# Kernel optimization log

Measured on AMD Instinct MI355X. Metric: run time of the kernel, lower is better.

The kernel has to match this reference:

```python
import jax, jax.numpy as jnp
import numpy as np

GROUPS = 9  # hardcoded in GTLModuleV1.forward


def setup_inputs() -> dict:
    key = jax.random.key(0)
    k1, k2, k3 = jax.random.split(key, 3)
    B, C, N, K = 4, 144, 16384, 16
    queryandkey = jax.random.normal(k1, (B, C, N), dtype=jnp.float32)
    value = jax.random.normal(k2, (B, C, N), dtype=jnp.float32)
    idx_knn = jax.random.randint(k3, (B, N, K), 0, N, dtype=jnp.int32)
    return {"queryandkey": queryandkey, "value": value, "idx_knn": idx_knn}


def _gather_neighbours(x, idx_flat, B, G, d, N, K):
    # x: (B, G, d, N); idx_flat: (B, 1, 1, N*K) -> (B, G, d, N, K)
    g = jnp.take_along_axis(x, jnp.broadcast_to(idx_flat, (B, G, d, N * K)), axis=3)
    return g.reshape(B, G, d, N, K)


def reference(queryandkey, value, idx_knn):
    B, C, N = queryandkey.shape
    K = idx_knn.shape[-1]
    G = GROUPS
    d = C // G  # Cl = C (Cnl = 0 in GTLModuleV1)

    q = queryandkey.reshape(B, G, d, N)          # LocalQuery == LocalKey source
    v = value.reshape(B, G, d, N)
    idx_flat = idx_knn.reshape(B, 1, 1, N * K)

    key_g = _gather_neighbours(q, idx_flat, B, G, d, N, K)  # (B,G,d,N,K)
    val_g = _gather_neighbours(v, idx_flat, B, G, d, N, K)  # (B,G,d,N,K)

    # LocalAtt = sum_d Q * K_gathered, softmax over neighbors
    att = jnp.einsum('bgdn,bgdnk->bgnk', q, key_g)
    att = jax.nn.softmax(att, axis=-1)                       # (B,G,N,K)

    # attention centrality: scatter_add of attention weights onto neighbor ids
    cent = jnp.zeros((B, G, N), dtype=att.dtype).at[
        jnp.arange(B)[:, None, None, None],
        jnp.arange(G)[None, :, None, None],
        idx_knn[:, None, :, :],
    ].add(att)                                               # (B,G,N)

    # weighted aggregation of gathered values
    feat = jnp.einsum('bgnk,bgdnk->bgdn', att, val_g).reshape(B, C, N)
    return feat, cent
```

## Files before the change

kernel.cpp:

```cpp
#include <hip/hip_runtime.h>
#include <hip/hip_fp16.h>

#define BATCH 4
#define CHAN  144
#define NPTS  16384
#define KNN   16
#define GRP   9
#define DIM   16
#define ROWU  (GRP * DIM)
#define PCHUNK 21
#define NPAIR (BATCH * GRP)

#define TT 32

typedef __attribute__((ext_vector_type(2))) _Float16 h2v;
typedef __attribute__((ext_vector_type(4))) float    f4v;
typedef __attribute__((ext_vector_type(4))) int      i4v;
typedef __attribute__((ext_vector_type(4))) unsigned u4v;
__device__ __forceinline__ h2v as_h2(unsigned int u) {
  union { unsigned int u; h2v h; } c; c.u = u; return c.h;
}
__device__ __forceinline__ float2 h2f(unsigned u) {
  union { unsigned u; __half2 h; } c; c.u = u;
  return __half22float2(c.h);
}

template<int J>
__device__ __forceinline__ int ibcast(int v) {
  return __builtin_amdgcn_update_dpp(0, v, (J) * 0x55, 0xF, 0xF, true);
}
template<int C>
__device__ __forceinline__ float fxor(float x) {
  int r = __builtin_amdgcn_update_dpp(0, __builtin_bit_cast(int, x), C, 0xF, 0xF, true);
  return __builtin_bit_cast(float, r);
}

__global__ __launch_bounds__(256) void pack_qv_kernel(
    const float* __restrict__ q, const float* __restrict__ v,
    unsigned int* __restrict__ qvT) {
  __shared__ float tq[TT][TT + 1];
  __shared__ float tv[TT][TT + 1];
  const int b = blockIdx.z;
  const float* qb = q + (size_t)b * CHAN * NPTS;
  const float* vb = v + (size_t)b * CHAN * NPTS;
  unsigned int* out = qvT + (size_t)b * NPTS * ROWU;
  const int n0 = blockIdx.x * TT;
  const int c0 = blockIdx.y * TT;
  const int t = threadIdx.x;

  {
    const int cl = t >> 3, nq = (t & 7) * 4;
    const int c = c0 + cl;
    if (c < CHAN) {
      const float4 a = *(const float4*)&qb[(size_t)c * NPTS + n0 + nq];
      tq[cl][nq + 0] = a.x; tq[cl][nq + 1] = a.y;
      tq[cl][nq + 2] = a.z; tq[cl][nq + 3] = a.w;
      const float4 w = *(const float4*)&vb[(size_t)c * NPTS + n0 + nq];
      tv[cl][nq + 0] = w.x; tv[cl][nq + 1] = w.y;
      tv[cl][nq + 2] = w.z; tv[cl][nq + 3] = w.w;
    }
  }
  __syncthreads();
  {
    const int nl = t >> 3, cq = (t & 7) * 4;
    const int c = c0 + cq;
    if (c < CHAN) {
      const int g = c >> 4, r = c & 15;
      __half2 k01 = __halves2half2(__float2half_rn(tq[cq + 0][nl]),
                                   __float2half_rn(tq[cq + 1][nl]));
      __half2 v01 = __halves2half2(__float2half_rn(tv[cq + 0][nl]),
                                   __float2half_rn(tv[cq + 1][nl]));
      __half2 k23 = __halves2half2(__float2half_rn(tq[cq + 2][nl]),
                                   __float2half_rn(tq[cq + 3][nl]));
      __half2 v23 = __halves2half2(__float2half_rn(tv[cq + 2][nl]),
                                   __float2half_rn(tv[cq + 3][nl]));
      *(uint4*)&out[(size_t)(n0 + nl) * ROWU + g * 16 + r] =
          make_uint4(*(unsigned int*)&k01, *(unsigned int*)&v01,
                     *(unsigned int*)&k23, *(unsigned int*)&v23);
    }
  }
}

__global__ __launch_bounds__(512, 4) void gtl_kernel(
    const unsigned int* __restrict__ qvT,
    const int*   __restrict__ idx,
    float* __restrict__ feat,
    float* __restrict__ part)
{
  const int i = blockIdx.x;
  const int x = i & 7, sblk = i >> 3;
  if (sblk >= 94 + ((x & 1) ^ 1)) return;
  int pair, chunk;
  if (sblk < 84) { pair = x + 8 * (sblk / PCHUNK); chunk = sblk % PCHUNK; }
  else           { pair = 32 + (x >> 1); chunk = (sblk - 84) + 11 * (x & 1); }
  const int b = pair / GRP;
  const int g = pair - b * GRP;

  __shared__ float lcent[NPTS];
  const int tid = threadIdx.x;

  f4v* l4 = (f4v*)lcent;
  #pragma unroll
  for (int ii = 0; ii < NPTS / 4 / 512; ++ii)
    l4[ii * 512 + tid] = (f4v){0.f, 0.f, 0.f, 0.f};
  __syncthreads();

  const int ngroups = 6 + (chunk < 2 ? 1 : 0);
  const int gstart  = 6 * chunk + (chunk < 2 ? chunk : 2);

  const int lane = tid & 63;
  const int wv   = tid >> 6;
  const int slot = lane >> 2;
  const int d    = lane & 3;

  const char* qvb  = (const char*)qvT + (size_t)b * NPTS * (ROWU * 4);
  const char* idxB = (const char*)idx + (size_t)b * NPTS * (KNN * 4);
  const unsigned laneB  = (unsigned)(g * 64 + d * 16);
  const unsigned idxoff = (unsigned)(d * 16);

  int n = gstart * 128 + wv * 16 + slot;
  i4v idq; u4v qq;
  asm volatile("global_load_dwordx4 %0, %1, %2"
               : "=v"(idq) : "v"((unsigned)n * 64u + idxoff), "s"(idxB));
  asm volatile("global_load_dwordx4 %0, %1, %2"
               : "=v"(qq) : "v"((unsigned)n * (ROWU * 4u) + laneB), "s"(qvb));
  asm volatile("s_waitcnt vmcnt(0)" ::: "memory");
  __builtin_amdgcn_sched_barrier(0);

  for (int it = 0; it < ngroups; ++it) {
    const h2v q01 = as_h2(qq.x);
    const h2v q23 = as_h2(qq.z);

    u4v kvA[8], kvB[8];
#define GISS(DST, K)                                                         \
    {                                                                        \
      const int mk = ibcast<((K) >> 2)>(                                     \
          ((K) & 3) == 0 ? idq.x : ((K) & 3) == 1 ? idq.y                    \
                         : ((K) & 3) == 2 ? idq.z : idq.w);                  \
      const unsigned vo = (unsigned)mk * (ROWU * 4u) + laneB;                \
      asm volatile("global_load_dwordx4 %0, %1, %2"                          \
                   : "=v"(DST) : "v"(vo), "s"(qvb));                         \
    }
    GISS(kvA[0], 0)  GISS(kvA[1], 1)  GISS(kvA[2], 2)  GISS(kvA[3], 3)
    GISS(kvA[4], 4)  GISS(kvA[5], 5)  GISS(kvA[6], 6)  GISS(kvA[7], 7)
    GISS(kvB[0], 8)  GISS(kvB[1], 9)  GISS(kvB[2], 10) GISS(kvB[3], 11)
    GISS(kvB[4], 12) GISS(kvB[5], 13) GISS(kvB[6], 14) GISS(kvB[7], 15)
#undef GISS

    const int itn = (it + 1 < ngroups) ? it + 1 : it;
    const int nn = (gstart + itn) * 128 + wv * 16 + slot;
    i4v idqn; u4v qqn;
    asm volatile("global_load_dwordx4 %0, %1, %2"
                 : "=v"(idqn) : "v"((unsigned)nn * 64u + idxoff), "s"(idxB));
    asm volatile("global_load_dwordx4 %0, %1, %2"
                 : "=v"(qqn) : "v"((unsigned)nn * (ROWU * 4u) + laneB), "s"(qvb));

    asm volatile("s_waitcnt vmcnt(10)" ::: "memory");
    __builtin_amdgcn_sched_barrier(0);

    float kp[4] = {0.f, 0.f, 0.f, 0.f};
    float sum = 0.f, a0 = 0.f, a1 = 0.f, a2 = 0.f, a3 = 0.f;
#define CSTEP(V, K)                                                          \
    {                                                                        \
      float s = __builtin_amdgcn_fdot2(as_h2((V).x), q01, 0.f, false);       \
      s = __builtin_amdgcn_fdot2(as_h2((V).z), q23, s, false);               \
      s += fxor<0xB1>(s);                                                    \
      s += fxor<0x4E>(s);                                                    \
      const float e = __expf(s);                                             \
      sum += e;                                                              \
      kp[(K) & 3] = (d == ((K) >> 2)) ? e : kp[(K) & 3];                     \
      const float2 v01 = h2f((V).y);                                         \
      const float2 v23 = h2f((V).w);                                         \
      a0 += e * v01.x; a1 += e * v01.y; a2 += e * v23.x; a3 += e * v23.y;    \
    }
    CSTEP(kvA[0], 0)  CSTEP(kvA[1], 1)  CSTEP(kvA[2], 2)  CSTEP(kvA[3], 3)
    CSTEP(kvA[4], 4)  CSTEP(kvA[5], 5)  CSTEP(kvA[6], 6)  CSTEP(kvA[7], 7)

    asm volatile("s_waitcnt vmcnt(2)" ::: "memory");
    __builtin_amdgcn_sched_barrier(0);
    CSTEP(kvB[0], 8)  CSTEP(kvB[1], 9)  CSTEP(kvB[2], 10) CSTEP(kvB[3], 11)
    CSTEP(kvB[4], 12) CSTEP(kvB[5], 13) CSTEP(kvB[6], 14) CSTEP(kvB[7], 15)
#undef CSTEP

    const float inv = 1.f / sum;

    atomicAdd(&lcent[idq.x], kp[0] * inv);
    atomicAdd(&lcent[idq.y], kp[1] * inv);
    atomicAdd(&lcent[idq.z], kp[2] * inv);
    atomicAdd(&lcent[idq.w], kp[3] * inv);

    float* fb = feat + ((size_t)b * CHAN + g * DIM + 4 * d) * NPTS + n;
    __builtin_nontemporal_store(a0 * inv, fb);
    __builtin_nontemporal_store(a1 * inv, fb + NPTS);
    __builtin_nontemporal_store(a2 * inv, fb + 2 * NPTS);
    __builtin_nontemporal_store(a3 * inv, fb + 3 * NPTS);

    asm volatile("s_waitcnt vmcnt(4)" ::: "memory");
    __builtin_amdgcn_sched_barrier(0);

    n = nn; idq = idqn; qq = qqn;
  }
  asm volatile("s_waitcnt vmcnt(0)" ::: "memory");
  __builtin_amdgcn_sched_barrier(0);

  __syncthreads();
  f4v* p4 = (f4v*)(part + ((size_t)pair * PCHUNK + chunk) * NPTS);
  #pragma unroll
  for (int i2 = 0; i2 < NPTS / 4 / 512; ++i2) {
    const int j = (i2 * 512 + tid + chunk * 512) & 4095;
    __builtin_nontemporal_store(l4[j], &p4[j]);
  }
}

__global__ __launch_bounds__(256) void reduce_cent_kernel(
    const float* __restrict__ part, float* __restrict__ cent) {
  const int t = blockIdx.x * 256 + threadIdx.x;
  const int bg = t >> 12;
  const int m4 = (t & 4095) << 2;
  const f4v* p = (const f4v*)(part + ((size_t)bg * PCHUNK) * NPTS + m4);
  f4v s = (f4v){0.f, 0.f, 0.f, 0.f};
  #pragma unroll
  for (int i = 0; i < PCHUNK; ++i) {
    f4v xv = __builtin_nontemporal_load(&p[(size_t)i * (NPTS / 4)]);
    s += xv;
  }
  *(f4v*)(cent + (size_t)bg * NPTS + m4) = s;
}

extern "C" void kernel_launch(void* const* d_in, const int* in_sizes, int n_in,
                              void* d_out, int out_size, void* d_ws, size_t ws_size,
                              hipStream_t stream) {
  const float* q   = (const float*)d_in[0];
  const float* v   = (const float*)d_in[1];
  const int*   idx = (const int*)d_in[2];

  float* feat = (float*)d_out;
  float* cent = feat + (size_t)BATCH * CHAN * NPTS;

  unsigned int* qvT = (unsigned int*)d_ws;
  float* part = (float*)(qvT + (size_t)BATCH * NPTS * ROWU);

  dim3 tg(NPTS / TT, (CHAN + TT - 1) / TT, BATCH);
  pack_qv_kernel<<<tg, 256, 0, stream>>>(q, v, qvT);

  gtl_kernel<<<760, 512, 0, stream>>>(qvT, idx, feat, part);

  reduce_cent_kernel<<<(NPAIR * NPTS / 4) / 256, 256, 0, stream>>>(part, cent);
}
```

Baseline: 210.5 us.

## Split GTL into group-pair kernel and separate ninth-group kernel

```diff
diff --git a/kernel.cpp b/kernel.cpp
--- a/kernel.cpp
+++ b/kernel.cpp
@@ -7,8 +7,9 @@
 #define KNN   16
 #define GRP   9
 #define DIM   16
-#define ROWU  (GRP * DIM)
-#define PCHUNK 21
+#define ROWU2 160
+#define PCHA  16
+#define PCHB  32
 #define NPAIR (BATCH * GRP)
 
 #define TT 32
@@ -43,7 +44,7 @@
   const int b = blockIdx.z;
   const float* qb = q + (size_t)b * CHAN * NPTS;
   const float* vb = v + (size_t)b * CHAN * NPTS;
-  unsigned int* out = qvT + (size_t)b * NPTS * ROWU;
+  unsigned int* out = qvT + (size_t)b * NPTS * ROWU2;
   const int n0 = blockIdx.x * TT;
   const int c0 = blockIdx.y * TT;
   const int t = threadIdx.x;
@@ -65,7 +66,6 @@
     const int nl = t >> 3, cq = (t & 7) * 4;
     const int c = c0 + cq;
     if (c < CHAN) {
-      const int g = c >> 4, r = c & 15;
       __half2 k01 = __halves2half2(__float2half_rn(tq[cq + 0][nl]),
                                    __float2half_rn(tq[cq + 1][nl]));
       __half2 v01 = __halves2half2(__float2half_rn(tv[cq + 0][nl]),
@@ -74,60 +74,56 @@
                                    __float2half_rn(tq[cq + 3][nl]));
       __half2 v23 = __halves2half2(__float2half_rn(tv[cq + 2][nl]),
                                    __float2half_rn(tv[cq + 3][nl]));
-      *(uint4*)&out[(size_t)(n0 + nl) * ROWU + g * 16 + r] =
+      *(uint4*)&out[(size_t)(n0 + nl) * ROWU2 + c] =
           make_uint4(*(unsigned int*)&k01, *(unsigned int*)&v01,
                      *(unsigned int*)&k23, *(unsigned int*)&v23);
     }
   }
 }
 
-__global__ __launch_bounds__(512, 4) void gtl_kernel(
+__global__ __launch_bounds__(512, 4) void gtl_pair_kernel(
     const unsigned int* __restrict__ qvT,
     const int*   __restrict__ idx,
     float* __restrict__ feat,
-    float* __restrict__ part)
+    float* __restrict__ partA)
 {
   const int i = blockIdx.x;
   const int x = i & 7, sblk = i >> 3;
-  if (sblk >= 94 + ((x & 1) ^ 1)) return;
-  int pair, chunk;
-  if (sblk < 84) { pair = x + 8 * (sblk / PCHUNK); chunk = sblk % PCHUNK; }
-  else           { pair = 32 + (x >> 1); chunk = (sblk - 84) + 11 * (x & 1); }
-  const int b = pair / GRP;
-  const int g = pair - b * GRP;
-
-  __shared__ float lcent[NPTS];
+  const int PU = x + 8 * (sblk >> 4);
+  const int chunk = sblk & 15;
+  const int b = PU >> 2, j = PU & 3;
+
+  extern __shared__ float lcent[];
   const int tid = threadIdx.x;
 
   f4v* l4 = (f4v*)lcent;
   #pragma unroll
-  for (int ii = 0; ii < NPTS / 4 / 512; ++ii)
+  for (int ii = 0; ii < 2 * NPTS / 4 / 512; ++ii)
     l4[ii * 512 + tid] = (f4v){0.f, 0.f, 0.f, 0.f};
   __syncthreads();
-
-  const int ngroups = 6 + (chunk < 2 ? 1 : 0);
-  const int gstart  = 6 * chunk + (chunk < 2 ? chunk : 2);
 
   const int lane = tid & 63;
   const int wv   = tid >> 6;
-  const int slot = lane >> 2;
-  const int d    = lane & 3;
-
-  const char* qvb  = (const char*)qvT + (size_t)b * NPTS * (ROWU * 4);
+  const int slot = lane >> 3;
+  const int e    = lane & 7;
+  const int gh   = e >> 2;
+  const int d    = e & 3;
+
+  const char* qvb  = (const char*)qvT + (size_t)b * NPTS * (ROWU2 * 4);
   const char* idxB = (const char*)idx + (size_t)b * NPTS * (KNN * 4);
-  const unsigned laneB  = (unsigned)(g * 64 + d * 16);
+  const unsigned laneB  = (unsigned)(j * 128 + e * 16);
   const unsigned idxoff = (unsigned)(d * 16);
 
-  int n = gstart * 128 + wv * 16 + slot;
+  int n = chunk * 1024 + wv * 8 + slot;
   i4v idq; u4v qq;
   asm volatile("global_load_dwordx4 %0, %1, %2"
                : "=v"(idq) : "v"((unsigned)n * 64u + idxoff), "s"(idxB));
   asm volatile("global_load_dwordx4 %0, %1, %2"
-               : "=v"(qq) : "v"((unsigned)n * (ROWU * 4u) + laneB), "s"(qvb));
+               : "=v"(qq) : "v"((unsigned)n * (ROWU2 * 4u) + laneB), "s"(qvb));
   asm volatile("s_waitcnt vmcnt(0)" ::: "memory");
   __builtin_amdgcn_sched_barrier(0);
 
-  for (int it = 0; it < ngroups; ++it) {
+  for (int it = 0; it < 16; ++it) {
     const h2v q01 = as_h2(qq.x);
     const h2v q23 = as_h2(qq.z);
 
@@ -137,7 +133,7 @@
       const int mk = ibcast<((K) >> 2)>(                                     \
           ((K) & 3) == 0 ? idq.x : ((K) & 3) == 1 ? idq.y                    \
                          : ((K) & 3) == 2 ? idq.z : idq.w);                  \
-      const unsigned vo = (unsigned)mk * (ROWU * 4u) + laneB;                \
+      const unsigned vo = (unsigned)mk * (ROWU2 * 4u) + laneB;               \
       asm volatile("global_load_dwordx4 %0, %1, %2"                          \
                    : "=v"(DST) : "v"(vo), "s"(qvb));                         \
     }
@@ -147,13 +143,13 @@
     GISS(kvB[4], 12) GISS(kvB[5], 13) GISS(kvB[6], 14) GISS(kvB[7], 15)
 #undef GISS
 
-    const int itn = (it + 1 < ngroups) ? it + 1 : it;
-    const int nn = (gstart + itn) * 128 + wv * 16 + slot;
+    const int itn = (it + 1 < 16) ? it + 1 : it;
+    const int nn = chunk * 1024 + itn * 64 + wv * 8 + slot;
     i4v idqn; u4v qqn;
     asm volatile("global_load_dwordx4 %0, %1, %2"
                  : "=v"(idqn) : "v"((unsigned)nn * 64u + idxoff), "s"(idxB));
     asm volatile("global_load_dwordx4 %0, %1, %2"
-                 : "=v"(qqn) : "v"((unsigned)nn * (ROWU * 4u) + laneB), "s"(qvb));
+                 : "=v"(qqn) : "v"((unsigned)nn * (ROWU2 * 4u) + laneB), "s"(qvb));
 
     asm volatile("s_waitcnt vmcnt(10)" ::: "memory");
     __builtin_amdgcn_sched_barrier(0);
@@ -166,12 +162,12 @@
       s = __builtin_amdgcn_fdot2(as_h2((V).z), q23, s, false);               \
       s += fxor<0xB1>(s);                                                    \
       s += fxor<0x4E>(s);                                                    \
-      const float e = __expf(s);                                             \
-      sum += e;                                                              \
-      kp[(K) & 3] = (d == ((K) >> 2)) ? e : kp[(K) & 3];                     \
+      const float e2 = __expf(s);                                            \
+      sum += e2;                                                             \
+      kp[(K) & 3] = (d == ((K) >> 2)) ? e2 : kp[(K) & 3];                    \
       const float2 v01 = h2f((V).y);                                         \
       const float2 v23 = h2f((V).w);                                         \
-      a0 += e * v01.x; a1 += e * v01.y; a2 += e * v23.x; a3 += e * v23.y;    \
+      a0 += e2 * v01.x; a1 += e2 * v01.y; a2 += e2 * v23.x; a3 += e2 * v23.y;\
     }
     CSTEP(kvA[0], 0)  CSTEP(kvA[1], 1)  CSTEP(kvA[2], 2)  CSTEP(kvA[3], 3)
     CSTEP(kvA[4], 4)  CSTEP(kvA[5], 5)  CSTEP(kvA[6], 6)  CSTEP(kvA[7], 7)
@@ -184,12 +180,136 @@
 
     const float inv = 1.f / sum;
 
+    float* lc = lcent + gh * NPTS;
+    atomicAdd(&lc[idq.x], kp[0] * inv);
+    atomicAdd(&lc[idq.y], kp[1] * inv);
+    atomicAdd(&lc[idq.z], kp[2] * inv);
+    atomicAdd(&lc[idq.w], kp[3] * inv);
+
+    float* fb = feat + ((size_t)b * CHAN + (2 * j + gh) * DIM + 4 * d) * NPTS + n;
+    __builtin_nontemporal_store(a0 * inv, fb);
+    __builtin_nontemporal_store(a1 * inv, fb + NPTS);
+    __builtin_nontemporal_store(a2 * inv, fb + 2 * NPTS);
+    __builtin_nontemporal_store(a3 * inv, fb + 3 * NPTS);
+
+    asm volatile("s_waitcnt vmcnt(4)" ::: "memory");
+    __builtin_amdgcn_sched_barrier(0);
+    n = nn; idq = idqn; qq = qqn;
+  }
+  asm volatile("s_waitcnt vmcnt(0)" ::: "memory");
+  __builtin_amdgcn_sched_barrier(0);
+
+  __syncthreads();
+  f4v* p4 = (f4v*)(partA + ((size_t)(PU * PCHA + chunk) * 2) * NPTS);
+  #pragma unroll
+  for (int i2 = 0; i2 < 2 * NPTS / 4 / 512; ++i2) {
+    const int j2 = (i2 * 512 + tid + chunk * 512) & 8191;
+    __builtin_nontemporal_store(l4[j2], &p4[j2]);
+  }
+}
+
+__global__ __launch_bounds__(512, 4) void gtl_g8_kernel(
+    const unsigned int* __restrict__ qvT,
+    const int*   __restrict__ idx,
+    float* __restrict__ feat,
+    float* __restrict__ partB)
+{
+  const int i = blockIdx.x;
+  const int x = i & 7, sblk = i >> 3;
+  const int b = x >> 1;
+  const int chunk = sblk + 16 * (x & 1);
+
+  __shared__ float lcent[NPTS];
+  const int tid = threadIdx.x;
+  f4v* l4 = (f4v*)lcent;
+  #pragma unroll
+  for (int ii = 0; ii < NPTS / 4 / 512; ++ii)
+    l4[ii * 512 + tid] = (f4v){0.f, 0.f, 0.f, 0.f};
+  __syncthreads();
+
+  const int NG = 4;
+  const int gstart = chunk * NG;
+
+  const int lane = tid & 63;
+  const int wv   = tid >> 6;
+  const int slot = lane >> 2;
+  const int d    = lane & 3;
+
+  const char* qvb  = (const char*)qvT + (size_t)b * NPTS * (ROWU2 * 4);
+  const char* idxB = (const char*)idx + (size_t)b * NPTS * (KNN * 4);
+  const unsigned laneB  = (unsigned)(8 * 64 + d * 16);
+  const unsigned idxoff = (unsigned)(d * 16);
+
+  int n = gstart * 128 + wv * 16 + slot;
+  i4v idq; u4v qq;
+  asm volatile("global_load_dwordx4 %0, %1, %2"
+               : "=v"(idq) : "v"((unsigned)n * 64u + idxoff), "s"(idxB));
+  asm volatile("global_load_dwordx4 %0, %1, %2"
+               : "=v"(qq) : "v"((unsigned)n * (ROWU2 * 4u) + laneB), "s"(qvb));
+  asm volatile("s_waitcnt vmcnt(0)" ::: "memory");
+  __builtin_amdgcn_sched_barrier(0);
+
+  for (int it = 0; it < NG; ++it) {
+    const h2v q01 = as_h2(qq.x);
+    const h2v q23 = as_h2(qq.z);
+
+    u4v kvA[8], kvB[8];
+#define GISS(DST, K)                                                         \
+    {                                                                        \
+      const int mk = ibcast<((K) >> 2)>(                                     \
+          ((K) & 3) == 0 ? idq.x : ((K) & 3) == 1 ? idq.y                    \
+                         : ((K) & 3) == 2 ? idq.z : idq.w);                  \
+      const unsigned vo = (unsigned)mk * (ROWU2 * 4u) + laneB;               \
+      asm volatile("global_load_dwordx4 %0, %1, %2"                          \
+                   : "=v"(DST) : "v"(vo), "s"(qvb));                         \
+    }
+    GISS(kvA[0], 0)  GISS(kvA[1], 1)  GISS(kvA[2], 2)  GISS(kvA[3], 3)
+    GISS(kvA[4], 4)  GISS(kvA[5], 5)  GISS(kvA[6], 6)  GISS(kvA[7], 7)
+    GISS(kvB[0], 8)  GISS(kvB[1], 9)  GISS(kvB[2], 10) GISS(kvB[3], 11)
+    GISS(kvB[4], 12) GISS(kvB[5], 13) GISS(kvB[6], 14) GISS(kvB[7], 15)
+#undef GISS
+
+    const int itn = (it + 1 < NG) ? it + 1 : it;
+    const int nn = (gstart + itn) * 128 + wv * 16 + slot;
+    i4v idqn; u4v qqn;
+    asm volatile("global_load_dwordx4 %0, %1, %2"
+                 : "=v"(idqn) : "v"((unsigned)nn * 64u + idxoff), "s"(idxB));
+    asm volatile("global_load_dwordx4 %0, %1, %2"
+                 : "=v"(qqn) : "v"((unsigned)nn * (ROWU2 * 4u) + laneB), "s"(qvb));
+
+    asm volatile("s_waitcnt vmcnt(10)" ::: "memory");
+    __builtin_amdgcn_sched_barrier(0);
+
+    float kp[4] = {0.f, 0.f, 0.f, 0.f};
+    float sum = 0.f, a0 = 0.f, a1 = 0.f, a2 = 0.f, a3 = 0.f;
+#define CSTEP(V, K)                                                          \
+    {                                                                        \
+      float s = __builtin_amdgcn_fdot2(as_h2((V).x), q01, 0.f, false);       \
+      s = __builtin_amdgcn_fdot2(as_h2((V).z), q23, s, false);               \
+      s += fxor<0xB1>(s);                                                    \
+      s += fxor<0x4E>(s);                                                    \
+      const float e2 = __expf(s);                                            \
+      sum += e2;                                                             \
+      kp[(K) & 3] = (d == ((K) >> 2)) ? e2 : kp[(K) & 3];                    \
+      const float2 v01 = h2f((V).y);                                         \
+      const float2 v23 = h2f((V).w);                                         \
+      a0 += e2 * v01.x; a1 += e2 * v01.y; a2 += e2 * v23.x; a3 += e2 * v23.y;\
+    }
+    CSTEP(kvA[0], 0)  CSTEP(kvA[1], 1)  CSTEP(kvA[2], 2)  CSTEP(kvA[3], 3)
+    CSTEP(kvA[4], 4)  CSTEP(kvA[5], 5)  CSTEP(kvA[6], 6)  CSTEP(kvA[7], 7)
+    asm volatile("s_waitcnt vmcnt(2)" ::: "memory");
+    __builtin_amdgcn_sched_barrier(0);
+    CSTEP(kvB[0], 8)  CSTEP(kvB[1], 9)  CSTEP(kvB[2], 10) CSTEP(kvB[3], 11)
+    CSTEP(kvB[4], 12) CSTEP(kvB[5], 13) CSTEP(kvB[6], 14) CSTEP(kvB[7], 15)
+#undef CSTEP
+
+    const float inv = 1.f / sum;
     atomicAdd(&lcent[idq.x], kp[0] * inv);
     atomicAdd(&lcent[idq.y], kp[1] * inv);
     atomicAdd(&lcent[idq.z], kp[2] * inv);
     atomicAdd(&lcent[idq.w], kp[3] * inv);
 
-    float* fb = feat + ((size_t)b * CHAN + g * DIM + 4 * d) * NPTS + n;
+    float* fb = feat + ((size_t)b * CHAN + 8 * DIM + 4 * d) * NPTS + n;
     __builtin_nontemporal_store(a0 * inv, fb);
     __builtin_nontemporal_store(a1 * inv, fb + NPTS);
     __builtin_nontemporal_store(a2 * inv, fb + 2 * NPTS);
@@ -197,32 +317,39 @@
 
     asm volatile("s_waitcnt vmcnt(4)" ::: "memory");
     __builtin_amdgcn_sched_barrier(0);
-
     n = nn; idq = idqn; qq = qqn;
   }
   asm volatile("s_waitcnt vmcnt(0)" ::: "memory");
   __builtin_amdgcn_sched_barrier(0);
 
   __syncthreads();
-  f4v* p4 = (f4v*)(part + ((size_t)pair * PCHUNK + chunk) * NPTS);
+  f4v* p4 = (f4v*)(partB + (size_t)(b * PCHB + chunk) * NPTS);
   #pragma unroll
   for (int i2 = 0; i2 < NPTS / 4 / 512; ++i2) {
-    const int j = (i2 * 512 + tid + chunk * 512) & 4095;
-    __builtin_nontemporal_store(l4[j], &p4[j]);
+    const int j2 = (i2 * 512 + tid + chunk * 128) & 4095;
+    __builtin_nontemporal_store(l4[j2], &p4[j2]);
   }
 }
 
 __global__ __launch_bounds__(256) void reduce_cent_kernel(
-    const float* __restrict__ part, float* __restrict__ cent) {
+    const float* __restrict__ partA, const float* __restrict__ partB,
+    float* __restrict__ cent) {
   const int t = blockIdx.x * 256 + threadIdx.x;
   const int bg = t >> 12;
   const int m4 = (t & 4095) << 2;
-  const f4v* p = (const f4v*)(part + ((size_t)bg * PCHUNK) * NPTS + m4);
+  const int b = bg / GRP, g = bg - b * GRP;
   f4v s = (f4v){0.f, 0.f, 0.f, 0.f};
-  #pragma unroll
-  for (int i = 0; i < PCHUNK; ++i) {
-    f4v xv = __builtin_nontemporal_load(&p[(size_t)i * (NPTS / 4)]);
-    s += xv;
+  if (g < 8) {
+    const int PU = b * 4 + (g >> 1), gh = g & 1;
+    const f4v* p = (const f4v*)(partA + ((size_t)(PU * PCHA) * 2 + gh) * NPTS + m4);
+    #pragma unroll
+    for (int i = 0; i < PCHA; ++i)
+      s += __builtin_nontemporal_load(&p[(size_t)i * 2 * (NPTS / 4)]);
+  } else {
+    const f4v* p = (const f4v*)(partB + (size_t)(b * PCHB) * NPTS + m4);
+    #pragma unroll
+    for (int i = 0; i < PCHB; ++i)
+      s += __builtin_nontemporal_load(&p[(size_t)i * (NPTS / 4)]);
   }
   *(f4v*)(cent + (size_t)bg * NPTS + m4) = s;
 }
@@ -238,12 +365,17 @@
   float* cent = feat + (size_t)BATCH * CHAN * NPTS;
 
   unsigned int* qvT = (unsigned int*)d_ws;
-  float* part = (float*)(qvT + (size_t)BATCH * NPTS * ROWU);
+  float* partA = (float*)(qvT + (size_t)BATCH * NPTS * ROWU2);
+  float* partB = partA + (size_t)16 * PCHA * 2 * NPTS;
 
   dim3 tg(NPTS / TT, (CHAN + TT - 1) / TT, BATCH);
   pack_qv_kernel<<<tg, 256, 0, stream>>>(q, v, qvT);
 
-  gtl_kernel<<<760, 512, 0, stream>>>(qvT, idx, feat, part);
-
-  reduce_cent_kernel<<<(NPAIR * NPTS / 4) / 256, 256, 0, stream>>>(part, cent);
-}
+  gtl_pair_kernel<<<256, 512, 2 * NPTS * sizeof(float), stream>>>(
+      qvT, idx, feat, partA);
+
+  gtl_g8_kernel<<<128, 512, 0, stream>>>(qvT, idx, feat, partB);
+
+  reduce_cent_kernel<<<(NPAIR * NPTS / 4) / 256, 256, 0, stream>>>(
+      partA, partB, cent);
+}
```

Result: no change. 210.2 us (-0.1%).
